# Kernel tuning notes

Hardware: AMD Instinct MI355X
Metric: run time of the kernel (lower is better)

## Reference

```python
import jax, jax.numpy as jnp
import numpy as np

QLEN, MLEN, BSZ, DM, NH, DH, DI = 512, 512, 8, 1024, 16, 64, 4096
KLEN = QLEN + MLEN
EPS = 1e-5
NEG = -1e30


def layer_norm(x, g, b):
    mu = jnp.mean(x, axis=-1, keepdims=True)
    var = jnp.mean(jnp.square(x - mu), axis=-1, keepdims=True)
    return (x - mu) * jax.lax.rsqrt(var + EPS) * g + b


def rel_shift(x):
    # x: [qlen, rlen, bsz, n_head] -> Transformer-XL relative shift
    q, r, b, n = x.shape
    zp = jnp.zeros((q, 1, b, n), x.dtype)
    xp = jnp.concatenate([zp, x], axis=1).reshape(r + 1, q, b, n)
    return xp[1:].reshape(q, r, b, n)


def setup_inputs() -> dict:
    key = jax.random.key(0)
    ks = jax.random.split(key, 12)
    inp = {
        "w": jax.random.normal(ks[0], (QLEN, BSZ, DM), jnp.float32),
        "r": jax.random.normal(ks[1], (KLEN, DM), jnp.float32),
        "mems": jax.random.normal(ks[2], (MLEN, BSZ, DM), jnp.float32),
        "w_qkv": jax.random.normal(ks[3], (DM, 3 * NH * DH), jnp.float32) * 0.02,
        "w_r": jax.random.normal(ks[4], (DM, NH * DH), jnp.float32) * 0.02,
        "w_o": jax.random.normal(ks[5], (NH * DH, DM), jnp.float32) * 0.02,
        "r_w_bias": jax.random.normal(ks[6], (NH, DH), jnp.float32) * 0.02,
        "r_r_bias": jax.random.normal(ks[7], (NH, DH), jnp.float32) * 0.02,
        "ln1_g": jnp.ones((DM,), jnp.float32),
        "ln1_b": jnp.zeros((DM,), jnp.float32),
        "ff_w1": jax.random.normal(ks[8], (DM, DI), jnp.float32) * 0.02,
        "ff_b1": jnp.zeros((DI,), jnp.float32),
        "ff_w2": jax.random.normal(ks[9], (DI, DM), jnp.float32) * 0.02,
        "ff_b2": jnp.zeros((DM,), jnp.float32),
        "ln2_g": jnp.ones((DM,), jnp.float32),
        "ln2_b": jnp.zeros((DM,), jnp.float32),
    }
    # causal mask with memory: query i (global pos MLEN+i) cannot attend to j > MLEN+i
    i = jnp.arange(QLEN)[:, None]
    j = jnp.arange(KLEN)[None, :]
    inp["attn_mask"] = j > (i + MLEN)
    return inp


def reference(w, r, mems, attn_mask, w_qkv, w_r, w_o, r_w_bias, r_r_bias,
              ln1_g, ln1_b, ff_w1, ff_b1, ff_w2, ff_b2, ln2_g, ln2_b):
    qlen, bsz = w.shape[0], w.shape[1]
    scale = 1.0 / (DH ** 0.5)
    cat = jnp.concatenate([mems, w], axis=0)                 # [klen, b, d]
    klen = cat.shape[0]
    heads = cat @ w_qkv                                      # [klen, b, 3*H*D]
    hq, hk, hv = jnp.split(heads, 3, axis=-1)
    hq = hq[-qlen:].reshape(qlen, bsz, NH, DH)
    hk = hk.reshape(klen, bsz, NH, DH)
    hv = hv.reshape(klen, bsz, NH, DH)
    r_head_k = (r @ w_r).reshape(klen, NH, DH)               # [rlen, H, D]

    AC = jnp.einsum('ibnd,jbnd->ijbn', hq + r_w_bias, hk)
    BD = rel_shift(jnp.einsum('ibnd,jnd->ijbn', hq + r_r_bias, r_head_k))
    score = (AC + BD) * scale                                # [q, k, b, h]
    score = jnp.where(attn_mask[:, :, None, None], NEG, score)
    prob = jax.nn.softmax(score, axis=1)
    vec = jnp.einsum('ijbn,jbnd->ibnd', prob, hv).reshape(qlen, bsz, NH * DH)
    attn_out = vec @ w_o
    h = layer_norm(w + attn_out, ln1_g, ln1_b)               # post-LN
    ff = jax.nn.relu(h @ ff_w1 + ff_b1) @ ff_w2 + ff_b2
    return layer_norm(h + ff, ln2_g, ln2_b)
```

## Files before the change

### kernel.cpp

```cpp
#include <hip/hip_runtime.h>
#include <hip/hip_bf16.h>

#define QLEN 512
#define MLEN 512
#define KLEN 1024
#define BSZ 8
#define DM 1024
#define NH 16
#define DH 64
#define DI 4096
#define NEGF (-1e30f)
#define HM_PART ((size_t)8388608)

typedef unsigned short u16;
typedef __attribute__((ext_vector_type(8))) short short8;
typedef __attribute__((ext_vector_type(4))) short s16x4;
typedef __attribute__((ext_vector_type(4))) float f32x4;
typedef __attribute__((ext_vector_type(4))) unsigned int u32x4;

__device__ __forceinline__ float bf2f(u16 u) {
    union { unsigned i; float f; } x; x.i = ((unsigned)u) << 16; return x.f;
}
__device__ __forceinline__ u16 f2bf(float f) {
    __hip_bfloat16 h = __float2bfloat16(f);
    return *reinterpret_cast<u16*>(&h);
}
__device__ __forceinline__ float4 ldg4(const float* p) {
    return *reinterpret_cast<const float4*>(p);
}
__device__ __forceinline__ void gload16(const void* g, void* l) {
    __builtin_amdgcn_global_load_lds(
        (const __attribute__((address_space(1))) void*)g,
        (__attribute__((address_space(3))) void*)l, 16, 0, 0);
}

__global__ __launch_bounds__(256) void cast_all(
    const float* __restrict__ mems, const float* __restrict__ w,
    const float* __restrict__ r, u16* __restrict__ catB, u16* __restrict__ rB)
{
    int idx = (blockIdx.x * 256 + threadIdx.x) * 4;
    const float* src;
    u16* dst;
    if (idx < 8388608) {
        src = (idx < 4194304) ? (mems + idx) : (w + idx - 4194304);
        dst = catB + idx;
    } else {
        int i2 = idx - 8388608;
        if (i2 >= 1048576) return;
        src = r + i2;
        dst = rB + i2;
    }
    float4 v = ldg4(src);
    u16 o[4] = { f2bf(v.x), f2bf(v.y), f2bf(v.z), f2bf(v.w) };
    *reinterpret_cast<uint2*>(dst) = *reinterpret_cast<uint2*>(o);
}

__device__ __forceinline__ void tr32(
    const float* __restrict__ W, u16* __restrict__ WT, int K, int N, int k0, int n0)
{
    __shared__ float tile[32][33];
    const int tx = threadIdx.x & 31, ty = threadIdx.x >> 5;
    #pragma unroll
    for (int j = 0; j < 4; ++j)
        tile[ty + j * 8][tx] = W[(size_t)(k0 + ty + j * 8) * N + n0 + tx];
    __syncthreads();
    #pragma unroll
    for (int j = 0; j < 4; ++j)
        WT[(size_t)(n0 + ty + j * 8) * K + k0 + tx] = f2bf(tile[tx][ty + j * 8]);
}

__global__ __launch_bounds__(256) void transpose_all(
    const float* __restrict__ w_qkv, u16* __restrict__ qkvT,
    const float* __restrict__ w_r,   u16* __restrict__ wrT,
    const float* __restrict__ w_o,   u16* __restrict__ woT,
    const float* __restrict__ ffw1,  u16* __restrict__ f1T,
    const float* __restrict__ ffw2,  u16* __restrict__ f2T)
{
    int id = blockIdx.x;
    if (id < 3072)       { int l = id;        tr32(w_qkv, qkvT, 1024, 3072, (l / 96) * 32, (l % 96) * 32); }
    else if (id < 4096)  { int l = id - 3072; tr32(w_r,   wrT,  1024, 1024, (l / 32) * 32, (l % 32) * 32); }
    else if (id < 5120)  { int l = id - 4096; tr32(w_o,   woT,  1024, 1024, (l / 32) * 32, (l % 32) * 32); }
    else if (id < 9216)  { int l = id - 5120; tr32(ffw1,  f1T,  1024, 4096, (l / 128) * 32, (l % 128) * 32); }
    else                 { int l = id - 9216; tr32(ffw2,  f2T,  4096, 1024, (l / 32) * 32, (l % 32) * 32); }
}

__global__ __launch_bounds__(256) void v_transpose(
    const u16* __restrict__ Vhm, u16* __restrict__ Vg)
{
    const int bn = blockIdx.x;
    const int kt = blockIdx.y;
    const int t = threadIdx.x;
    __shared__ u16 L[64 * 64];

    #pragma unroll
    for (int rep = 0; rep < 2; ++rep) {
        int idx = t + rep * 256;
        int key = idx >> 3, dc = (idx & 7) * 8;
        short8 v = *reinterpret_cast<const short8*>(
            &Vhm[((size_t)bn * 1024 + kt * 64 + key) * 64 + dc]);
        *reinterpret_cast<short8*>((char*)L + key * 128 + ((dc * 2) ^ ((key & 7) << 4))) = v;
    }
    __syncthreads();
    #pragma unroll
    for (int rep = 0; rep < 2; ++rep) {
        int idx = t + rep * 256;
        int d = idx >> 3, kc = (idx & 7) * 8;
        short8 o;
        #pragma unroll
        for (int e = 0; e < 8; ++e)
            o[e] = *(const short*)((char*)L + (kc + e) * 128 + ((d * 2) ^ (((kc + e) & 7) << 4)));
        *reinterpret_cast<short8*>(&Vg[((size_t)(bn * 64 + d)) * KLEN + kt * 64 + kc]) = o;
    }
}

template<bool BIAS, bool RELU, int OUT>
__global__ __launch_bounds__(256) void gemm_mfma(
    const u16* __restrict__ A, const u16* __restrict__ BT,
    const float* __restrict__ bias,
    float* __restrict__ Cf, u16* __restrict__ Cb,
    int M, int N, int K, int lda, int ldb)
{
    __shared__ u16 As[128 * 64];
    __shared__ u16 Bs[128 * 64];
    const int bm = blockIdx.y * 128, bn = blockIdx.x * 128;
    const int z = blockIdx.z;
    A  += (size_t)z * K;
    BT += (size_t)z * K;
    const size_t zoff = (size_t)z * M * N;
    const int t = threadIdx.x;
    const int w = t >> 6, l = t & 63, lg = l >> 4, lq = l & 15;
    const int wm = (w >> 1) * 64, wn = (w & 1) * 64;
    const int r8 = l >> 3, slot = l & 7;
    const int gcol = (slot * 16) ^ (r8 << 4);

    f32x4 acc[4][4];
    #pragma unroll
    for (int x = 0; x < 4; ++x)
        #pragma unroll
        for (int y = 0; y < 4; ++y)
            acc[x][y] = (f32x4){0.f, 0.f, 0.f, 0.f};

    const int swzr = (lq & 7) << 4;

    for (int k0 = 0; k0 < K; k0 += 64) {
        __syncthreads();
        #pragma unroll
        for (int it = 0; it < 4; ++it) {
            const int base_row = w * 8 + it * 32;
            gload16((const char*)A + (((size_t)(bm + base_row + r8) * lda + k0) << 1) + gcol,
                    (char*)As + base_row * 128);
            gload16((const char*)BT + (((size_t)(bn + base_row + r8) * ldb + k0) << 1) + gcol,
                    (char*)Bs + base_row * 128);
        }
        __syncthreads();
        #pragma unroll
        for (int ks = 0; ks < 2; ++ks) {
            const int cb = (ks * 64 + 16 * lg) ^ swzr;
            short8 af[4], bf_[4];
            #pragma unroll
            for (int x = 0; x < 4; ++x)
                af[x] = *reinterpret_cast<const short8*>((char*)As + (wm + 16 * x + lq) * 128 + cb);
            #pragma unroll
            for (int y = 0; y < 4; ++y)
                bf_[y] = *reinterpret_cast<const short8*>((char*)Bs + (wn + 16 * y + lq) * 128 + cb);
            #pragma unroll
            for (int x = 0; x < 4; ++x)
                #pragma unroll
                for (int y = 0; y < 4; ++y)
                    acc[x][y] = __builtin_amdgcn_mfma_f32_16x16x32_bf16(af[x], bf_[y], acc[x][y], 0, 0, 0);
        }
    }
    const int nn = ((bn + wn) >> 6) & 15;
    #pragma unroll
    for (int x = 0; x < 4; ++x) {
        #pragma unroll
        for (int y = 0; y < 4; ++y) {
            const int col = bn + wn + 16 * y + lq;
            #pragma unroll
            for (int r = 0; r < 4; ++r) {
                const int row = bm + wm + 16 * x + 4 * lg + r;
                float v = acc[x][y][r];
                if constexpr (BIAS) { if (z == 0) v += bias[col]; }
                if constexpr (RELU) v = fmaxf(v, 0.f);
                if constexpr (OUT == 0) Cf[zoff + (size_t)row * N + col] = v;
                else if constexpr (OUT == 1) Cb[zoff + (size_t)row * N + col] = f2bf(v);
                else
                    Cb[((size_t)nn * 1024 + row) * 64 + 16 * y + lq] = f2bf(v);
            }
        }
    }
}

template<bool BIAS, bool RELU, int OUT>
__global__ __launch_bounds__(512, 2) void gemm_deep(
    const u16* __restrict__ A, const u16* __restrict__ BT,
    const float* __restrict__ bias,
    float* __restrict__ Cf, u16* __restrict__ Cb,
    int M, int N, int K, int lda, int ldb)
{
    __shared__ u16 lds[3 * 24576];
    const int bm = blockIdx.y * 256, bn = blockIdx.x * 128;
    const int z = blockIdx.z;
    A  += (size_t)z * K;
    BT += (size_t)z * K;
    const size_t zoff = (size_t)z * M * N;
    const int t = threadIdx.x;
    const int w = t >> 6, l = t & 63, lg = l >> 4, lq = l & 15;
    const int wm = (w >> 1) * 64;
    const int wn = (w & 1) * 64;
    const int srow = t >> 3, slot = t & 7;
    const int gcol = (slot * 16) ^ ((srow & 7) << 4);
    const int swzr = (lq & 7) << 4;

    auto stage_tile = [&](int kt, int buf) {
        const int k0 = kt * 64;
        char* Ab = (char*)lds + buf * 49152 + w * 1024;
        char* Bb = (char*)lds + buf * 49152 + 32768 + w * 1024;
        #pragma unroll
        for (int i = 0; i < 4; ++i)
            gload16((const char*)A + (((size_t)(bm + i * 64 + srow) * lda + k0) << 1) + gcol,
                    Ab + i * 8192);
        #pragma unroll
        for (int i = 0; i < 2; ++i)
            gload16((const char*)BT + (((size_t)(bn + i * 64 + srow) * ldb + k0) << 1) + gcol,
                    Bb + i * 8192);
    };

    f32x4 acc[4][4];
    #pragma unroll
    for (int x = 0; x < 4; ++x)
        #pragma unroll
        for (int y = 0; y < 4; ++y)
            acc[x][y] = (f32x4){0.f, 0.f, 0.f, 0.f};

    const int NT = K >> 6;
    stage_tile(0, 0);
    stage_tile(1, 1);

    for (int kt = 0; kt < NT; ++kt) {
        if (kt < NT - 1) asm volatile("s_waitcnt vmcnt(6)" ::: "memory");
        else             asm volatile("s_waitcnt vmcnt(0)" ::: "memory");
        __builtin_amdgcn_s_barrier();
        __builtin_amdgcn_sched_barrier(0);
        if (kt + 2 < NT) stage_tile(kt + 2, (kt + 2) % 3);

        const char* Ab = (const char*)lds + (kt % 3) * 49152;
        const char* Bb = Ab + 32768;
        #pragma unroll
        for (int ks = 0; ks < 2; ++ks) {
            const int cb = (ks * 64 + 16 * lg) ^ swzr;
            short8 af[4], bf_[4];
            #pragma unroll
            for (int x = 0; x < 4; ++x)
                af[x] = *reinterpret_cast<const short8*>(Ab + (wm + 16 * x + lq) * 128 + cb);
            #pragma unroll
            for (int y = 0; y < 4; ++y)
                bf_[y] = *reinterpret_cast<const short8*>(Bb + (wn + 16 * y + lq) * 128 + cb);
            __builtin_amdgcn_s_setprio(1);
            #pragma unroll
            for (int x = 0; x < 4; ++x)
                #pragma unroll
                for (int y = 0; y < 4; ++y)
                    acc[x][y] = __builtin_amdgcn_mfma_f32_16x16x32_bf16(af[x], bf_[y], acc[x][y], 0, 0, 0);
            __builtin_amdgcn_s_setprio(0);
        }
    }

    #pragma unroll
    for (int x = 0; x < 4; ++x) {
        #pragma unroll
        for (int y = 0; y < 4; ++y) {
            const int col = bn + wn + 16 * y + lq;
            #pragma unroll
            for (int r = 0; r < 4; ++r) {
                const int row = bm + wm + 16 * x + 4 * lg + r;
                float v = acc[x][y][r];
                if constexpr (BIAS) { if (z == 0) v += bias[col]; }
                if constexpr (RELU) v = fmaxf(v, 0.f);
                if constexpr (OUT == 0) Cf[zoff + (size_t)row * N + col] = v;
                else Cb[zoff + (size_t)row * N + col] = f2bf(v);
            }
        }
    }
}

template<bool BIAS, bool RELU, int OUT>
__global__ __launch_bounds__(512, 2) void gemm256(
    const u16* __restrict__ A, const u16* __restrict__ BT,
    const float* __restrict__ bias, u16* __restrict__ Cb,
    int N, int K, int lda, int ldb, int nbx)
{
    __shared__ u16 lds[2 * 32768];
    const int id = ((int)blockIdx.x % 8) * ((int)gridDim.x / 8) + (int)blockIdx.x / 8;
    int bm, bn;
    if constexpr (OUT == 2) {
        if (id < 64) { bm = 4096 + (id >> 2) * 256; bn = (id & 3) * 256; }
        else         { int j = id - 64; bm = (j >> 3) * 256; bn = 1024 + (j & 7) * 256; }
    } else {
        bm = (id / nbx) * 256; bn = (id % nbx) * 256;
    }
    const int t = threadIdx.x;
    const int w = t >> 6, l = t & 63, lg = l >> 4, lq = l & 15;
    const int wm = (w >> 2) * 128;
    const int wn = (w & 3) * 64;
    const int srow = t >> 3, slot = t & 7;
    const int gcol = (slot * 16) ^ ((srow & 7) << 4);
    const int swzr = (lq & 7) << 4;

    auto stage_unit = [&](int kt, char* buf, int u) {
        const int k0 = kt * 64;
        if (u < 2) {
            #pragma unroll
            for (int i = 0; i < 2; ++i) {
                int g = u * 2 + i;
                gload16((const char*)BT + (((size_t)(bn + g * 64 + srow) * ldb + k0) << 1) + gcol,
                        buf + 32768 + g * 8192 + w * 1024);
            }
        } else {
            #pragma unroll
            for (int i = 0; i < 2; ++i) {
                int g = (u - 2) + i * 2;
                gload16((const char*)A + (((size_t)(bm + g * 64 + srow) * lda + k0) << 1) + gcol,
                        buf + g * 8192 + w * 1024);
            }
        }
    };

    f32x4 acc[8][4];
    #pragma unroll
    for (int m = 0; m < 8; ++m)
        #pragma unroll
        for (int y = 0; y < 4; ++y)
            acc[m][y] = (f32x4){0.f, 0.f, 0.f, 0.f};

    const int NT = K >> 6;
    #pragma unroll
    for (int u = 0; u < 4; ++u) stage_unit(0, (char*)lds, u);

    for (int kt = 0; kt < NT; ++kt) {
        const char* Ab = (const char*)lds + (kt & 1) * 65536;
        const char* Bb = Ab + 32768;
        char* nbuf = (char*)lds + ((kt + 1) & 1) * 65536;
        const bool pf = (kt + 1 < NT);
        const int cb0 = (16 * lg) ^ swzr;
        const int cb1 = (64 + 16 * lg) ^ swzr;

        short8 bk0[4], bk1[4], a00[4], a01[4], a10[4], a11[4];

        asm volatile("s_waitcnt vmcnt(2)" ::: "memory");
        __builtin_amdgcn_s_barrier();
        __builtin_amdgcn_sched_barrier(0);
        #pragma unroll
        for (int y = 0; y < 4; ++y)
            bk0[y] = *reinterpret_cast<const short8*>(Bb + (wn + 16 * y + lq) * 128 + cb0);
        __builtin_amdgcn_sched_barrier(0);
        #pragma unroll
        for (int x = 0; x < 4; ++x)
            a00[x] = *reinterpret_cast<const short8*>(Ab + (wm + 16 * x + lq) * 128 + cb0);
        __builtin_amdgcn_sched_barrier(0);
        #pragma unroll
        for (int y = 0; y < 4; ++y)
            bk1[y] = *reinterpret_cast<const short8*>(Bb + (wn + 16 * y + lq) * 128 + cb1);
        __builtin_amdgcn_sched_barrier(0);
        #pragma unroll
        for (int x = 0; x < 4; ++x)
            a01[x] = *reinterpret_cast<const short8*>(Ab + (wm + 16 * x + lq) * 128 + cb1);
        __builtin_amdgcn_sched_barrier(0);
        if (pf) stage_unit(kt + 1, nbuf, 0);
        asm volatile("s_waitcnt lgkmcnt(8)" ::: "memory");
        __builtin_amdgcn_sched_barrier(0);
        __builtin_amdgcn_s_setprio(1);
        #pragma unroll
        for (int x = 0; x < 4; ++x)
            #pragma unroll
            for (int y = 0; y < 4; ++y)
                acc[x][y] = __builtin_amdgcn_mfma_f32_16x16x32_bf16(a00[x], bk0[y], acc[x][y], 0, 0, 0);
        __builtin_amdgcn_s_setprio(0);

        if (pf) asm volatile("s_waitcnt vmcnt(2)" ::: "memory");
        else    asm volatile("s_waitcnt vmcnt(0)" ::: "memory");
        __builtin_amdgcn_s_barrier();
        __builtin_amdgcn_sched_barrier(0);
        #pragma unroll
        for (int x = 0; x < 4; ++x)
            a10[x] = *reinterpret_cast<const short8*>(Ab + (wm + 64 + 16 * x + lq) * 128 + cb0);
        __builtin_amdgcn_sched_barrier(0);
        #pragma unroll
        for (int x = 0; x < 4; ++x)
            a11[x] = *reinterpret_cast<const short8*>(Ab + (wm + 64 + 16 * x + lq) * 128 + cb1);
        __builtin_amdgcn_sched_barrier(0);
        if (pf) stage_unit(kt + 1, nbuf, 1);
        asm volatile("s_waitcnt lgkmcnt(8)" ::: "memory");
        __builtin_amdgcn_sched_barrier(0);
        __builtin_amdgcn_s_setprio(1);
        #pragma unroll
        for (int x = 0; x < 4; ++x)
            #pragma unroll
            for (int y = 0; y < 4; ++y)
                acc[x][y] = __builtin_amdgcn_mfma_f32_16x16x32_bf16(a01[x], bk1[y], acc[x][y], 0, 0, 0);
        __builtin_amdgcn_s_setprio(0);

        __builtin_amdgcn_s_barrier();
        __builtin_amdgcn_sched_barrier(0);
        if (pf) stage_unit(kt + 1, nbuf, 2);
        asm volatile("s_waitcnt lgkmcnt(4)" ::: "memory");
        __builtin_amdgcn_sched_barrier(0);
        __builtin_amdgcn_s_setprio(1);
        #pragma unroll
        for (int x = 0; x < 4; ++x)
            #pragma unroll
            for (int y = 0; y < 4; ++y)
                acc[4 + x][y] = __builtin_amdgcn_mfma_f32_16x16x32_bf16(a10[x], bk0[y], acc[4 + x][y], 0, 0, 0);
        __builtin_amdgcn_s_setprio(0);

        __builtin_amdgcn_s_barrier();
        __builtin_amdgcn_sched_barrier(0);
        if (pf) stage_unit(kt + 1, nbuf, 3);
        asm volatile("s_waitcnt lgkmcnt(0)" ::: "memory");
        __builtin_amdgcn_sched_barrier(0);
        __builtin_amdgcn_s_setprio(1);
        #pragma unroll
        for (int x = 0; x < 4; ++x)
            #pragma unroll
            for (int y = 0; y < 4; ++y)
                acc[4 + x][y] = __builtin_amdgcn_mfma_f32_16x16x32_bf16(a11[x], bk1[y], acc[4 + x][y], 0, 0, 0);
        __builtin_amdgcn_s_setprio(0);
    }

    #pragma unroll
    for (int m = 0; m < 8; ++m) {
        #pragma unroll
        for (int y = 0; y < 4; ++y) {
            const int col = bn + wn + 16 * y + lq;
            #pragma unroll
            for (int r = 0; r < 4; ++r) {
                const int row = bm + wm + m * 16 + 4 * lg + r;
                float v = acc[m][y][r];
                if constexpr (BIAS) v += bias[col];
                if constexpr (RELU) v = fmaxf(v, 0.f);
                if constexpr (OUT == 2) {
                    const int part = col >> 10, nn = (col >> 6) & 15;
                    Cb[(size_t)part * HM_PART
                       + ((size_t)((row & 7) * 16 + nn) * 1024 + (row >> 3)) * 64
                       + (col & 63)] = f2bf(v);
                } else {
                    Cb[(size_t)row * N + col] = f2bf(v);
                }
            }
        }
    }
}

__global__ __launch_bounds__(512, 4) void attn_mfma(
    const u16* __restrict__ Hm,
    const u16* __restrict__ Vg,
    const u16* __restrict__ rhm,
    const float* __restrict__ rwb, const float* __restrict__ rrb,
    u16* __restrict__ vec)
{
    const int bnidx = blockIdx.x;
    const int b = bnidx >> 4;
    const int n = bnidx & 15;
    const int i0 = (3 - blockIdx.y) * 128;
    const int t = threadIdx.x;
    const int w = t >> 6;
    const int l = t & 63;
    const int lg = l >> 4, lq = l & 15;
    const int r8 = l >> 3, sl = l & 7;

    const u16* Qh = Hm;
    const u16* Kh = Hm + HM_PART;

    __shared__ u16 Ks[64 * 64];
    __shared__ u16 Vt[64 * 64];
    __shared__ u16 Rs[192 * 64];
    __shared__ u16 SbO[8 * 16 * 84];
    __shared__ u16 Ps[8 * 16 * 64];

    u16* SbW = SbO + w * 16 * 84;
    u16* PsW = Ps + w * 16 * 64;
    const int swzr = (lq & 7) << 4;
    const int stg_swz = (sl * 16) ^ (r8 << 4);
    const int lofs = l * 16;
    const int rbase = 384 - i0;
    const int ntiles = i0 / 64 + 10;

    auto kSrc = [&](int tile) {
        return (const char*)Kh + (((size_t)bnidx * 1024 + (tile << 6) + w * 8 + r8) * 64 << 1) + stg_swz;
    };
    auto vSrc = [&](int tile) {
        return (const char*)Vg + ((((size_t)bnidx * 64 + w * 8 + r8) * KLEN + (tile << 6)) << 1) + stg_swz;
    };
    auto rSrc = [&](int g) {
        int o = rbase + g * 64 + w * 8 + r8;
        o = o > (KLEN - 1) ? (KLEN - 1) : o;
        return (const char*)rhm + (((size_t)n * 1024 + o) * 64 << 1) + stg_swz;
    };

    short8 qw[2], qr[2];
    {
        const size_t qbase = ((size_t)bnidx * 1024 + MLEN + i0 + 16 * w + lq) * 64;
        #pragma unroll
        for (int ks = 0; ks < 2; ++ks) {
            short8 qv = *reinterpret_cast<const short8*>(&Qh[qbase + ks * 32 + 8 * lg]);
            short8 xw, xr;
            #pragma unroll
            for (int e = 0; e < 8; ++e) {
                float f = bf2f((u16)qv[e]);
                int d = ks * 32 + 8 * lg + e;
                xw[e] = (short)f2bf((f + rwb[n * 64 + d]) * 0.125f);
                xr[e] = (short)f2bf((f + rrb[n * 64 + d]) * 0.125f);
            }
            qw[ks] = xw; qr[ks] = xr;
        }
    }

    float m_run = NEGF, l_run = 0.f;
    f32x4 acc[4];
    #pragma unroll
    for (int df = 0; df < 4; ++df) acc[df] = (f32x4){0.f, 0.f, 0.f, 0.f};

    const int s0 = 112 - 16 * w;

    u32x4 kreg = *reinterpret_cast<const u32x4*>(kSrc(0));
    u32x4 vreg = *reinterpret_cast<const u32x4*>(vSrc(0));
    u32x4 rr0  = *reinterpret_cast<const u32x4*>(rSrc(0));
    u32x4 rr1  = *reinterpret_cast<const u32x4*>(rSrc(1));
    u32x4 rr2  = *reinterpret_cast<const u32x4*>(rSrc(2));

    for (int tile = 0; tile < ntiles; ++tile) {
        const int j0 = tile << 6;
        __builtin_amdgcn_s_barrier();
        __builtin_amdgcn_sched_barrier(0);
        *reinterpret_cast<u32x4*>((char*)Ks + w * 1024 + lofs) = kreg;
        *reinterpret_cast<u32x4*>((char*)Vt + w * 1024 + lofs) = vreg;
        if (tile == 0) {
            *reinterpret_cast<u32x4*>((char*)Rs + 0 * 8192 + w * 1024 + lofs) = rr0;
            *reinterpret_cast<u32x4*>((char*)Rs + 1 * 8192 + w * 1024 + lofs) = rr1;
            *reinterpret_cast<u32x4*>((char*)Rs + 2 * 8192 + w * 1024 + lofs) = rr2;
        } else {
            *reinterpret_cast<u32x4*>((char*)Rs + ((tile + 2) % 3) * 8192 + w * 1024 + lofs) = rr0;
        }
        if (tile + 1 < ntiles) {
            kreg = *reinterpret_cast<const u32x4*>(kSrc(tile + 1));
            vreg = *reinterpret_cast<const u32x4*>(vSrc(tile + 1));
            rr0  = *reinterpret_cast<const u32x4*>(rSrc(tile + 3));
        }
        asm volatile("s_waitcnt lgkmcnt(0)" ::: "memory");
        __builtin_amdgcn_s_barrier();
        __builtin_amdgcn_sched_barrier(0);

        const int bmax = i0 + 16 * w + 15 + MLEN - j0;
        if (bmax < 0) continue;

        __builtin_amdgcn_s_setprio(1);
        #pragma unroll
        for (int ff = 0; ff < 5; ++ff) {
            const int olf = s0 + 16 * ff;
            const int srowb = ((tile + (olf >> 6)) % 3) * 64 + (olf & 63);
            f32x4 d = (f32x4){0.f, 0.f, 0.f, 0.f};
            #pragma unroll
            for (int ks = 0; ks < 2; ++ks) {
                short8 a = *reinterpret_cast<const short8*>(
                    (char*)Rs + (srowb + lq) * 128 + ((ks * 64 + 16 * lg) ^ swzr));
                d = __builtin_amdgcn_mfma_f32_16x16x32_bf16(a, qr[ks], d, 0, 0, 0);
            }
            s16x4 pk;
            #pragma unroll
            for (int r = 0; r < 4; ++r) pk[r] = (short)f2bf(d[r]);
            *reinterpret_cast<s16x4*>(&SbW[lq * 84 + 16 * ff + 4 * lg]) = pk;
        }
        f32x4 dac[4];
        #pragma unroll
        for (int f = 0; f < 4; ++f) {
            f32x4 d = (f32x4){0.f, 0.f, 0.f, 0.f};
            #pragma unroll
            for (int ks = 0; ks < 2; ++ks) {
                short8 a = *reinterpret_cast<const short8*>(
                    (char*)Ks + (16 * f + lq) * 128 + ((ks * 64 + 16 * lg) ^ swzr));
                d = __builtin_amdgcn_mfma_f32_16x16x32_bf16(a, qw[ks], d, 0, 0, 0);
            }
            dac[f] = d;
        }
        __builtin_amdgcn_s_setprio(0);

        const bool fullTile = (i0 + 16 * w + MLEN - j0) >= 63;
        float sv[4][4];
        float mx = NEGF;
        if (fullTile) {
            #pragma unroll
            for (int f = 0; f < 4; ++f)
                #pragma unroll
                for (int r = 0; r < 4; ++r) {
                    int k = 16 * f + 4 * lg + r;
                    float x = dac[f][r] + bf2f(SbW[lq * 84 + k - lq + 15]);
                    sv[f][r] = x;
                    mx = fmaxf(mx, x);
                }
        } else {
            const int bound = i0 + 16 * w + lq + MLEN - j0;
            #pragma unroll
            for (int f = 0; f < 4; ++f)
                #pragma unroll
                for (int r = 0; r < 4; ++r) {
                    int k = 16 * f + 4 * lg + r;
                    float x = (k <= bound)
                        ? dac[f][r] + bf2f(SbW[lq * 84 + k - lq + 15]) : NEGF;
                    sv[f][r] = x;
                    mx = fmaxf(mx, x);
                }
        }
        mx = fmaxf(mx, __shfl_xor(mx, 16));
        mx = fmaxf(mx, __shfl_xor(mx, 32));
        const bool defer = (__all(mx <= m_run + 8.0f) != 0);
        const float m_new = defer ? m_run : fmaxf(m_run, mx);
        float ps = 0.f;
        #pragma unroll
        for (int f = 0; f < 4; ++f) {
            s16x4 pk;
            #pragma unroll
            for (int r = 0; r < 4; ++r) {
                float p = __expf(sv[f][r] - m_new);
                ps += p;
                pk[r] = (short)f2bf(p);
            }
            *reinterpret_cast<s16x4*>(
                (char*)PsW + lq * 128 + (((4 * f + lg) ^ ((lq & 7) << 1)) << 3)) = pk;
        }
        ps += __shfl_xor(ps, 16);
        ps += __shfl_xor(ps, 32);
        if (defer) {
            l_run += ps;
        } else {
            float alpha = __expf(m_run - m_new);
            l_run = l_run * alpha + ps;
            m_run = m_new;
            float alr[4];
            #pragma unroll
            for (int r = 0; r < 4; ++r) alr[r] = __shfl(alpha, 20 * lg + r);
            #pragma unroll
            for (int df = 0; df < 4; ++df)
                #pragma unroll
                for (int r = 0; r < 4; ++r) acc[df][r] *= alr[r];
        }

        __builtin_amdgcn_s_setprio(1);
        #pragma unroll
        for (int df = 0; df < 4; ++df) {
            f32x4 a = acc[df];
            #pragma unroll
            for (int ks = 0; ks < 2; ++ks) {
                short8 pa = *reinterpret_cast<const short8*>(
                    (char*)PsW + lq * 128 + ((ks * 64 + 16 * lg) ^ swzr));
                short8 vb = *reinterpret_cast<const short8*>(
                    (char*)Vt + (16 * df + lq) * 128 + ((ks * 64 + 16 * lg) ^ swzr));
                a = __builtin_amdgcn_mfma_f32_16x16x32_bf16(pa, vb, a, 0, 0, 0);
            }
            acc[df] = a;
        }
        __builtin_amdgcn_s_setprio(0);
    }

    float inv[4];
    #pragma unroll
    for (int r = 0; r < 4; ++r) inv[r] = 1.f / __shfl(l_run, 20 * lg + r);
    #pragma unroll
    for (int df = 0; df < 4; ++df) {
        #pragma unroll
        for (int r = 0; r < 4; ++r) {
            const int il = 16 * w + 4 * lg + r;
            float o = acc[df][r] * inv[r];
            vec[((size_t)((i0 + il) * BSZ + b)) * DM + n * 64 + 16 * df + lq] = f2bf(o);
        }
    }
}

template<int NRES, bool WB>
__global__ __launch_bounds__(256) void ln_res_kernel(
    const float* __restrict__ x, const float* __restrict__ res,
    const float* __restrict__ res2,
    const float* __restrict__ g, const float* __restrict__ bta,
    float* __restrict__ out, u16* __restrict__ outb)
{
    const int row = blockIdx.x;
    const int t = threadIdx.x;
    const int lane = t & 63, wv = t >> 6;
    __shared__ float red0[4], red1[4];

    float4 a = ldg4(&x[(size_t)row * DM + t * 4]);
    float4 b = ldg4(&res[(size_t)row * DM + t * 4]);
    float v0 = a.x + b.x, v1 = a.y + b.y, v2 = a.z + b.z, v3 = a.w + b.w;
    if constexpr (NRES == 2) {
        float4 c = ldg4(&res2[(size_t)row * DM + t * 4]);
        v0 += c.x; v1 += c.y; v2 += c.z; v3 += c.w;
    }
    float s = v0 + v1 + v2 + v3;
    #pragma unroll
    for (int o = 32; o; o >>= 1) s += __shfl_xor(s, o);
    if (lane == 0) red0[wv] = s;
    __syncthreads();
    float mu = (red0[0] + red0[1] + red0[2] + red0[3]) * (1.f / DM);
    float d0 = v0 - mu, d1 = v1 - mu, d2 = v2 - mu, d3 = v3 - mu;
    float q = d0*d0 + d1*d1 + d2*d2 + d3*d3;
    #pragma unroll
    for (int o = 32; o; o >>= 1) q += __shfl_xor(q, o);
    if (lane == 0) red1[wv] = q;
    __syncthreads();
    float var = (red1[0] + red1[1] + red1[2] + red1[3]) * (1.f / DM);
    float rs = rsqrtf(var + 1e-5f);
    float4 gv = ldg4(&g[t * 4]);
    float4 bv = ldg4(&bta[t * 4]);
    float o0 = d0 * rs * gv.x + bv.x;
    float o1 = d1 * rs * gv.y + bv.y;
    float o2 = d2 * rs * gv.z + bv.z;
    float o3 = d3 * rs * gv.w + bv.w;
    float4 o4 = make_float4(o0, o1, o2, o3);
    *reinterpret_cast<float4*>(&out[(size_t)row * DM + t * 4]) = o4;
    if constexpr (WB) {
        u16 ob[4] = { f2bf(o0), f2bf(o1), f2bf(o2), f2bf(o3) };
        *reinterpret_cast<uint2*>(&outb[(size_t)row * DM + t * 4]) = *reinterpret_cast<uint2*>(ob);
    }
}

extern "C" void kernel_launch(void* const* d_in, const int* in_sizes, int n_in,
                              void* d_out, int out_size, void* d_ws, size_t ws_size,
                              hipStream_t stream) {
    const float* w     = (const float*)d_in[0];
    const float* r     = (const float*)d_in[1];
    const float* mems  = (const float*)d_in[2];
    const float* w_qkv = (const float*)d_in[3];
    const float* w_r   = (const float*)d_in[4];
    const float* w_o   = (const float*)d_in[5];
    const float* rwb   = (const float*)d_in[6];
    const float* rrb   = (const float*)d_in[7];
    const float* ln1g  = (const float*)d_in[8];
    const float* ln1b  = (const float*)d_in[9];
    const float* ffw1  = (const float*)d_in[10];
    const float* ffb1  = (const float*)d_in[11];
    const float* ffw2  = (const float*)d_in[12];
    const float* ffb2  = (const float*)d_in[13];
    const float* ln2g  = (const float*)d_in[14];
    const float* ln2b  = (const float*)d_in[15];
    (void)in_sizes; (void)n_in; (void)out_size; (void)ws_size;

    char* p = (char*)d_ws;
    auto alloc = [&](size_t bytes) { char* q = p; p += (bytes + 255) & ~(size_t)255; return q; };
    u16* catB   = (u16*)alloc((size_t)8192 * 1024 * 2);
    u16* rB     = (u16*)alloc((size_t)1024 * 1024 * 2);
    u16* qkvT   = (u16*)alloc((size_t)3072 * 1024 * 2);
    u16* wrT    = (u16*)alloc((size_t)1024 * 1024 * 2);
    u16* woT    = (u16*)alloc((size_t)1024 * 1024 * 2);
    u16* f1T    = (u16*)alloc((size_t)4096 * 1024 * 2);
    u16* f2T    = (u16*)alloc((size_t)1024 * 4096 * 2);
    u16* headsHm= (u16*)alloc((size_t)3 * HM_PART * 2);
    u16* rhkHm  = (u16*)alloc((size_t)1024 * 1024 * 2);
    u16* vec    = (u16*)alloc((size_t)4096 * 1024 * 2);
    u16* hB     = (u16*)alloc((size_t)4096 * 1024 * 2);
    u16* ff1    = (u16*)alloc((size_t)4096 * 4096 * 2);
    float* hF   = (float*)alloc((size_t)4096 * 1024 * 4);

    u16* Vg = catB;
    float* attn_out = (float*)ff1;
    float* ff2 = (float*)headsHm;
    float* outp = (float*)d_out;

    cast_all<<<9216, 256, 0, stream>>>(mems, w, r, catB, rB);
    transpose_all<<<13312, 256, 0, stream>>>(w_qkv, qkvT, w_r, wrT, w_o, woT,
                                             ffw1, f1T, ffw2, f2T);

    gemm256<false, false, 2><<<320, 512, 0, stream>>>(
        catB, qkvT, nullptr, headsHm, 3072, 1024, 1024, 1024, 0);
    v_transpose<<<dim3(128, 16), 256, 0, stream>>>(headsHm + 2 * HM_PART, Vg);
    gemm_mfma<false, false, 3><<<dim3(8, 8), 256, 0, stream>>>(
        rB, wrT, nullptr, nullptr, rhkHm, 1024, 1024, 1024, 1024, 1024);
    attn_mfma<<<dim3(BSZ * NH, QLEN / 128), 512, 0, stream>>>(
        headsHm, Vg, rhkHm, rwb, rrb, vec);
    gemm_mfma<false, false, 0><<<dim3(8, 32, 2), 256, 0, stream>>>(
        vec, woT, nullptr, attn_out, nullptr, 4096, 1024, 512, 1024, 1024);
    ln_res_kernel<2, true><<<4096, 256, 0, stream>>>(
        w, attn_out, attn_out + (size_t)4096 * 1024, ln1g, ln1b, hF, hB);
    gemm256<true, true, 1><<<256, 512, 0, stream>>>(
        hB, f1T, ffb1, ff1, 4096, 1024, 1024, 1024, 16);
    gemm_deep<true, false, 0><<<dim3(8, 16, 2), 512, 0, stream>>>(
        ff1, f2T, ffb2, ff2, nullptr, 4096, 1024, 2048, 4096, 4096);
    ln_res_kernel<2, false><<<4096, 256, 0, stream>>>(
        hF, ff2, ff2 + (size_t)4096 * 1024, ln2g, ln2b, outp, nullptr);
}
```

Baseline: 299.8 us.

## Fuse r-projection GEMM into QKV GEMM launch and store split-K partials as bf16

The separate r @ w_r GEMM launch is folded into the QKV gemm256 grid as 16 extra tiles, which write the rhkHm head-major layout directly. This removes one kernel launch and lets the small GEMM run alongside the large one. Split-K partial outputs of the w_o and ff_w2 GEMMs are now stored as bf16 instead of fp32, and the layer-norm kernels read bf16 residual partials, which halves the traffic for those intermediates. The cost is extra rounding of the partial sums before they are added.

```diff
diff --git a/kernel.cpp b/kernel.cpp
--- a/kernel.cpp
+++ b/kernel.cpp
@@ -170,7 +170,6 @@
                     acc[x][y] = __builtin_amdgcn_mfma_f32_16x16x32_bf16(af[x], bf_[y], acc[x][y], 0, 0, 0);
         }
     }
-    const int nn = ((bn + wn) >> 6) & 15;
     #pragma unroll
     for (int x = 0; x < 4; ++x) {
         #pragma unroll
@@ -183,9 +182,7 @@
                 if constexpr (BIAS) { if (z == 0) v += bias[col]; }
                 if constexpr (RELU) v = fmaxf(v, 0.f);
                 if constexpr (OUT == 0) Cf[zoff + (size_t)row * N + col] = v;
-                else if constexpr (OUT == 1) Cb[zoff + (size_t)row * N + col] = f2bf(v);
-                else
-                    Cb[((size_t)nn * 1024 + row) * 64 + 16 * y + lq] = f2bf(v);
+                else Cb[zoff + (size_t)row * N + col] = f2bf(v);
             }
         }
     }
@@ -288,14 +285,19 @@
 __global__ __launch_bounds__(512, 2) void gemm256(
     const u16* __restrict__ A, const u16* __restrict__ BT,
     const float* __restrict__ bias, u16* __restrict__ Cb,
-    int N, int K, int lda, int ldb, int nbx)
+    int N, int K, int lda, int ldb, int nbx,
+    const u16* __restrict__ A2, const u16* __restrict__ B2T,
+    u16* __restrict__ Cb2)
 {
     __shared__ u16 lds[2 * 32768];
     const int id = ((int)blockIdx.x % 8) * ((int)gridDim.x / 8) + (int)blockIdx.x / 8;
     int bm, bn;
+    bool isR = false;
     if constexpr (OUT == 2) {
-        if (id < 64) { bm = 4096 + (id >> 2) * 256; bn = (id & 3) * 256; }
-        else         { int j = id - 64; bm = (j >> 3) * 256; bn = 1024 + (j & 7) * 256; }
+        if (id >= 320)     { int j = id - 320; bm = (j >> 2) * 256; bn = (j & 3) * 256;
+                             isR = true; A = A2; BT = B2T; }
+        else if (id < 64)  { bm = 4096 + (id >> 2) * 256; bn = (id & 3) * 256; }
+        else               { int j = id - 64; bm = (j >> 3) * 256; bn = 1024 + (j & 7) * 256; }
     } else {
         bm = (id / nbx) * 256; bn = (id % nbx) * 256;
     }
@@ -439,10 +441,15 @@
                 if constexpr (BIAS) v += bias[col];
                 if constexpr (RELU) v = fmaxf(v, 0.f);
                 if constexpr (OUT == 2) {
-                    const int part = col >> 10, nn = (col >> 6) & 15;
-                    Cb[(size_t)part * HM_PART
-                       + ((size_t)((row & 7) * 16 + nn) * 1024 + (row >> 3)) * 64
-                       + (col & 63)] = f2bf(v);
+                    if (isR) {
+                        const int nn = (col >> 6) & 15;
+                        Cb2[((size_t)nn * 1024 + row) * 64 + (col & 63)] = f2bf(v);
+                    } else {
+                        const int part = col >> 10, nn = (col >> 6) & 15;
+                        Cb[(size_t)part * HM_PART
+                           + ((size_t)((row & 7) * 16 + nn) * 1024 + (row >> 3)) * 64
+                           + (col & 63)] = f2bf(v);
+                    }
                 } else {
                     Cb[(size_t)row * N + col] = f2bf(v);
                 }
@@ -677,8 +684,8 @@
 
 template<int NRES, bool WB>
 __global__ __launch_bounds__(256) void ln_res_kernel(
-    const float* __restrict__ x, const float* __restrict__ res,
-    const float* __restrict__ res2,
+    const float* __restrict__ x,
+    const u16* __restrict__ r0, const u16* __restrict__ r1,
     const float* __restrict__ g, const float* __restrict__ bta,
     float* __restrict__ out, u16* __restrict__ outb)
 {
@@ -687,12 +694,17 @@
     const int lane = t & 63, wv = t >> 6;
     __shared__ float red0[4], red1[4];
 
-    float4 a = ldg4(&x[(size_t)row * DM + t * 4]);
-    float4 b = ldg4(&res[(size_t)row * DM + t * 4]);
-    float v0 = a.x + b.x, v1 = a.y + b.y, v2 = a.z + b.z, v3 = a.w + b.w;
-    if constexpr (NRES == 2) {
-        float4 c = ldg4(&res2[(size_t)row * DM + t * 4]);
-        v0 += c.x; v1 += c.y; v2 += c.z; v3 += c.w;
+    const size_t base = (size_t)row * DM + t * 4;
+    float4 a = ldg4(&x[base]);
+    float v0 = a.x, v1 = a.y, v2 = a.z, v3 = a.w;
+    const u16* rs[2] = { r0, r1 };
+    #pragma unroll
+    for (int s = 0; s < NRES; ++s) {
+        uint2 u = *reinterpret_cast<const uint2*>(&rs[s][base]);
+        v0 += bf2f((u16)(u.x & 0xffff));
+        v1 += bf2f((u16)(u.x >> 16));
+        v2 += bf2f((u16)(u.y & 0xffff));
+        v3 += bf2f((u16)(u.y >> 16));
     }
     float s = v0 + v1 + v2 + v3;
     #pragma unroll
@@ -707,18 +719,18 @@
     if (lane == 0) red1[wv] = q;
     __syncthreads();
     float var = (red1[0] + red1[1] + red1[2] + red1[3]) * (1.f / DM);
-    float rs = rsqrtf(var + 1e-5f);
+    float rsq = rsqrtf(var + 1e-5f);
     float4 gv = ldg4(&g[t * 4]);
     float4 bv = ldg4(&bta[t * 4]);
-    float o0 = d0 * rs * gv.x + bv.x;
-    float o1 = d1 * rs * gv.y + bv.y;
-    float o2 = d2 * rs * gv.z + bv.z;
-    float o3 = d3 * rs * gv.w + bv.w;
+    float o0 = d0 * rsq * gv.x + bv.x;
+    float o1 = d1 * rsq * gv.y + bv.y;
+    float o2 = d2 * rsq * gv.z + bv.z;
+    float o3 = d3 * rsq * gv.w + bv.w;
     float4 o4 = make_float4(o0, o1, o2, o3);
-    *reinterpret_cast<float4*>(&out[(size_t)row * DM + t * 4]) = o4;
+    *reinterpret_cast<float4*>(&out[base]) = o4;
     if constexpr (WB) {
         u16 ob[4] = { f2bf(o0), f2bf(o1), f2bf(o2), f2bf(o3) };
-        *reinterpret_cast<uint2*>(&outb[(size_t)row * DM + t * 4]) = *reinterpret_cast<uint2*>(ob);
+        *reinterpret_cast<uint2*>(&outb[base]) = *reinterpret_cast<uint2*>(ob);
     }
 }
 
@@ -760,29 +772,28 @@
     float* hF   = (float*)alloc((size_t)4096 * 1024 * 4);
 
     u16* Vg = catB;
-    float* attn_out = (float*)ff1;
-    float* ff2 = (float*)headsHm;
+    u16* aoP = ff1;
+    u16* f2P = headsHm;
+    const size_t PSTR = (size_t)4096 * 1024;
     float* outp = (float*)d_out;
 
     cast_all<<<9216, 256, 0, stream>>>(mems, w, r, catB, rB);
     transpose_all<<<13312, 256, 0, stream>>>(w_qkv, qkvT, w_r, wrT, w_o, woT,
                                              ffw1, f1T, ffw2, f2T);
 
-    gemm256<false, false, 2><<<320, 512, 0, stream>>>(
-        catB, qkvT, nullptr, headsHm, 3072, 1024, 1024, 1024, 0);
+    gemm256<false, false, 2><<<336, 512, 0, stream>>>(
+        catB, qkvT, nullptr, headsHm, 3072, 1024, 1024, 1024, 0, rB, wrT, rhkHm);
     v_transpose<<<dim3(128, 16), 256, 0, stream>>>(headsHm + 2 * HM_PART, Vg);
-    gemm_mfma<false, false, 3><<<dim3(8, 8), 256, 0, stream>>>(
-        rB, wrT, nullptr, nullptr, rhkHm, 1024, 1024, 1024, 1024, 1024);
     attn_mfma<<<dim3(BSZ * NH, QLEN / 128), 512, 0, stream>>>(
         headsHm, Vg, rhkHm, rwb, rrb, vec);
-    gemm_mfma<false, false, 0><<<dim3(8, 32, 2), 256, 0, stream>>>(
-        vec, woT, nullptr, attn_out, nullptr, 4096, 1024, 512, 1024, 1024);
+    gemm_mfma<false, false, 1><<<dim3(8, 32, 2), 256, 0, stream>>>(
+        vec, woT, nullptr, nullptr, aoP, 4096, 1024, 512, 1024, 1024);
     ln_res_kernel<2, true><<<4096, 256, 0, stream>>>(
-        w, attn_out, attn_out + (size_t)4096 * 1024, ln1g, ln1b, hF, hB);
+        w, aoP, aoP + PSTR, ln1g, ln1b, hF, hB);
     gemm256<true, true, 1><<<256, 512, 0, stream>>>(
-        hB, f1T, ffb1, ff1, 4096, 1024, 1024, 1024, 16);
-    gemm_deep<true, false, 0><<<dim3(8, 16, 2), 512, 0, stream>>>(
-        ff1, f2T, ffb2, ff2, nullptr, 4096, 1024, 2048, 4096, 4096);
+        hB, f1T, ffb1, ff1, 4096, 1024, 1024, 1024, 16, nullptr, nullptr, nullptr);
+    gemm_deep<true, false, 1><<<dim3(8, 16, 2), 512, 0, stream>>>(
+        ff1, f2T, ffb2, nullptr, f2P, 4096, 1024, 2048, 4096, 4096);
     ln_res_kernel<2, false><<<4096, 256, 0, stream>>>(
-        hF, ff2, ff2 + (size_t)4096 * 1024, ln2g, ln2b, outp, nullptr);
-}
+        hF, f2P, f2P + PSTR, ln2g, ln2b, outp, nullptr);
+}
```

Measured after the change: 282.2 us. 5.9% less time.
